# Kernel optimization log

Hardware: AMD Instinct MI355X
Metric: run time of the kernel (lower is better)

Reference implementation:

```python
import jax, jax.numpy as jnp
import numpy as np

W_BIT = 4
G_SIZE = 128
HID = 4096
INTER = 11008
TOKS = (2, 2048)


def _dequant(qw, qz, scales, g_size):
    """Unpack int4 nibbles from int32 and dequantize: (w - zero) * scale.
    qw: [K, N//8] int32, qz: [K//g, N//8] int32, scales: [K//g, N] float.
    Returns dense weight [K, N] in scales.dtype."""
    K = qw.shape[0]
    shifts = (jnp.arange(8, dtype=jnp.int32) * 4)  # 8 nibbles per int32
    w = ((qw[:, :, None] >> shifts) & 0xF).reshape(K, -1).astype(scales.dtype)   # [K, N]
    z = ((qz[:, :, None] >> shifts) & 0xF).reshape(qz.shape[0], -1).astype(scales.dtype)  # [K//g, N]
    zr = jnp.repeat(z, g_size, axis=0)       # broadcast zero-points over group rows
    sr = jnp.repeat(scales, g_size, axis=0)  # broadcast scales over group rows
    return (w - zr) * sr


def setup_inputs() -> dict:
    key = jax.random.key(0)
    ks = jax.random.split(key, 7)
    B, S = TOKS
    x = jax.random.normal(ks[0], (B, S, HID), dtype=jnp.float32)
    imax = 2147483647
    qweight_gu = jax.random.randint(ks[1], (HID, 2 * INTER // 8), 0, imax, dtype=jnp.int32)
    qzeros_gu = jax.random.randint(ks[2], (HID // G_SIZE, 2 * INTER // 8), 0, imax, dtype=jnp.int32)
    scales_gu = jax.random.uniform(ks[3], (HID // G_SIZE, 2 * INTER), dtype=jnp.float32) * 0.01 + 1e-3
    qweight_dn = jax.random.randint(ks[4], (INTER, HID // 8), 0, imax, dtype=jnp.int32)
    qzeros_dn = jax.random.randint(ks[5], (INTER // G_SIZE, HID // 8), 0, imax, dtype=jnp.int32)
    scales_dn = jax.random.uniform(ks[6], (INTER // G_SIZE, HID), dtype=jnp.float32) * 0.01 + 1e-3
    return {"x": x, "qweight_gu": qweight_gu, "qzeros_gu": qzeros_gu, "scales_gu": scales_gu,
            "qweight_dn": qweight_dn, "qzeros_dn": qzeros_dn, "scales_dn": scales_dn}


def reference(x, qweight_gu, qzeros_gu, scales_gu, qweight_dn, qzeros_dn, scales_dn):
    # gate_up projection: x [B,S,H] @ W_gu [H, 2*I]
    W_gu = _dequant(qweight_gu, qzeros_gu, scales_gu, G_SIZE)
    gate_up = jnp.einsum('bsh,hi->bsi', x, W_gu)
    d = gate_up.shape[-1] // 2
    # SiluAndMul: silu(gate) * up
    h = jax.nn.silu(gate_up[..., :d]) * gate_up[..., d:]
    # down projection: h [B,S,I] @ W_dn [I, H]
    W_dn = _dequant(qweight_dn, qzeros_dn, scales_dn, G_SIZE)
    return jnp.einsum('bsi,ih->bsh', h, W_dn)
```

## Files before the change

kernel.cpp:

```cpp
#include <hip/hip_runtime.h>
#include <hip/hip_bf16.h>
#include <hip/hip_fp16.h>
#include <cstdint>
#include <cstddef>

#define AS1 __attribute__((address_space(1)))
#define AS3 __attribute__((address_space(3)))

constexpr int HIDC   = 4096;
constexpr int INTERC = 11008;
constexpr int NTOKC  = 4096;
constexpr int NWGU   = 2 * INTERC;

using f32x4 = __attribute__((ext_vector_type(4))) float;
using f16x8 = __attribute__((ext_vector_type(8))) _Float16;


__global__ void cvt_x_kernel(const float4* __restrict__ x, ushort4* __restrict__ xh, int n4) {
  int stride = gridDim.x * blockDim.x;
  for (int i = blockIdx.x * blockDim.x + threadIdx.x; i < n4; i += stride) {
    float4 v = x[i];
    ushort4 o;
    o.x = __builtin_bit_cast(unsigned short, __float2half(v.x));
    o.y = __builtin_bit_cast(unsigned short, __float2half(v.y));
    o.z = __builtin_bit_cast(unsigned short, __float2half(v.z));
    o.w = __builtin_bit_cast(unsigned short, __float2half(v.w));
    xh[i] = o;
  }
}

__global__ void repack_kernel(const uint32_t* __restrict__ qw, uint32_t* __restrict__ qt,
                              int kints, int Wn) {
  long total  = (long)Wn * kints;
  long stride = (long)gridDim.x * blockDim.x;
  for (long idx = blockIdx.x * (long)blockDim.x + threadIdx.x; idx < total; idx += stride) {
    int col = (int)(idx / kints);
    int kk  = (int)(idx - (long)col * kints);
    uint32_t ow[8] = {0, 0, 0, 0, 0, 0, 0, 0};
#pragma unroll
    for (int j = 0; j < 8; ++j) {
      uint32_t v = qw[(size_t)(kk * 8 + j) * Wn + col];
      const int pos = (j & 1) ? (4 + (j >> 1)) : (j >> 1);
#pragma unroll
      for (int jn = 0; jn < 8; ++jn)
        ow[jn] |= ((v >> (4 * jn)) & 0xFu) << (4 * pos);
    }
#pragma unroll
    for (int jn = 0; jn < 8; ++jn)
      qt[(size_t)(col * 8 + jn) * kints + kk] = ow[jn];
  }
}

__global__ void mktab_kernel(const uint32_t* __restrict__ qz, const float* __restrict__ sc,
                             uint2* __restrict__ tab, int total, int Nw) {
  int stride = gridDim.x * blockDim.x;
  for (int idx = blockIdx.x * blockDim.x + threadIdx.x; idx < total; idx += stride) {
    int g = idx / Nw, n = idx - g * Nw;
    uint32_t z = (qz[(size_t)g * (Nw >> 3) + (n >> 3)] >> ((n & 7) * 4)) & 0xFu;
    float s = sc[idx];
    uint32_t us = (uint32_t)__builtin_bit_cast(unsigned short, __float2half(s));
    uint32_t uc = (uint32_t)__builtin_bit_cast(unsigned short, __float2half(-s * (float)z));
    tab[idx] = make_uint2(us | (us << 16), uc | (uc << 16));
  }
}

template <int DUAL, int NT, int KINTS, int NWTOT, int NXT, int K>
__global__ __launch_bounds__(512, 2) void qgemm_kernel(
    const __half* __restrict__ A, const uint32_t* __restrict__ QT,
    const uint2* __restrict__ TAB, __half* __restrict__ Hout,
    float* __restrict__ Fout) {
  __shared__ __align__(16) char lds[131072];

  const int tid  = threadIdx.x;
  const int lane = tid & 63;
  const int w    = tid >> 6;
  const int wr   = w >> 2, wc = w & 3;
  const int fr   = lane & 15;
  const int fq   = lane >> 4;

  const int nwg8 = (int)gridDim.x >> 3;
  const int g2   = (blockIdx.x & 7) * nwg8 + ((int)blockIdx.x >> 3);
  const int mt   = g2 / NXT;
  const int nt   = g2 - mt * NXT;
  const int row0 = mt * 256;

  int a_src[4];
#pragma unroll
  for (int i = 0; i < 4; ++i) {
    int o = i * 8192 + tid * 16;
    int r = o >> 7;
    int b = (o & 127) ^ ((r & 7) << 4);
    a_src[i] = (row0 + r) * K + (b >> 1);
  }

  const int tc = tid >> 1, kh = tid & 1;
  int wcol;
  if (DUAL) {
    const int p = tc >> 5, mat = (tc >> 4) & 1, c16 = tc & 15;
    wcol = nt * 128 + p * 16 + c16 + mat * INTERC;
  } else {
    wcol = nt * 256 + tc;
  }
  const uint32_t* qbase = QT + (size_t)wcol * KINTS + kh * 4;
  const int boff = 32768 + tc * 128;
  const int bswz = (tc & 7) << 4;

  f32x4 acc[8][4] = {};

  auto stageA = [&](int kt, int buf) {
#pragma unroll
    for (int i = 0; i < 4; ++i)
      __builtin_amdgcn_global_load_lds((const AS1 uint32_t*)(A + a_src[i] + kt * 64),
                                       (AS3 uint32_t*)(lds + buf * 65536 + i * 8192 + w * 1024),
                                       16, 0, 0);
  };

  auto dequantB = [&](uint4 q, uint2 tz, int buf) {
    const __half2 s2 = __builtin_bit_cast(__half2, tz.x);
    const __half2 c2 = __builtin_bit_cast(__half2, tz.y);
    const __half2 k1024 = __builtin_bit_cast(__half2, 0x64006400u);
    char* bd = lds + buf * 65536 + boff;
    uint32_t qq[4] = {q.x, q.y, q.z, q.w};
#pragma unroll
    for (int ii = 0; ii < 4; ++ii) {
      uint32_t r[4];
#pragma unroll
      for (int i = 0; i < 4; ++i) {
        uint32_t pr = ((qq[ii] >> (4 * i)) & 0x000F000Fu) | 0x64006400u;
        __half2 t  = __hsub2(__builtin_bit_cast(__half2, pr), k1024);
        __half2 wv = __hfma2(t, s2, c2);
        r[i] = __builtin_bit_cast(uint32_t, wv);
      }
      *(uint4*)(bd + ((kh * 64 + ii * 16) ^ bswz)) = make_uint4(r[0], r[1], r[2], r[3]);
    }
  };

  auto compute = [&](int buf) {
    const char* base = lds + buf * 65536;
#pragma unroll
    for (int kk = 0; kk < 2; ++kk) {
      const int bb = (((kk << 2) | fq) ^ (fr & 7)) << 4;
      f16x8 av[8], bv[4];
#pragma unroll
      for (int mi = 0; mi < 8; ++mi)
        av[mi] = *(const f16x8*)(base + (wr * 128 + mi * 16 + fr) * 128 + bb);
#pragma unroll
      for (int ni = 0; ni < 4; ++ni)
        bv[ni] = *(const f16x8*)(base + 32768 + (wc * 64 + ni * 16 + fr) * 128 + bb);
      __builtin_amdgcn_s_setprio(1);
#pragma unroll
      for (int mi = 0; mi < 8; ++mi)
#pragma unroll
        for (int ni = 0; ni < 4; ++ni)
          acc[mi][ni] = __builtin_amdgcn_mfma_f32_16x16x32_f16(av[mi], bv[ni], acc[mi][ni], 0, 0, 0);
      __builtin_amdgcn_s_setprio(0);
    }
  };

  uint4 q  = *(const uint4*)qbase;
  uint2 tz = TAB[(size_t)wcol];
  stageA(0, 0);
  dequantB(q, tz, 0);
  __syncthreads();
  q  = *(const uint4*)(qbase + 8);
  tz = TAB[(size_t)(1 >> 1) * NWTOT + wcol];

  int cur = 0;
#pragma unroll 1
  for (int kt = 0; kt < NT; ++kt) {
    if (kt + 1 < NT) {
      stageA(kt + 1, cur ^ 1);
      dequantB(q, tz, cur ^ 1);
    }
    if (kt + 2 < NT) {
      q  = *(const uint4*)(qbase + (kt + 2) * 8);
      tz = TAB[(size_t)((kt + 2) >> 1) * NWTOT + wcol];
    }
    compute(cur);
    __syncthreads();
    cur ^= 1;
  }

  if (DUAL) {
#pragma unroll
    for (int mi = 0; mi < 8; ++mi) {
      const int rr = row0 + wr * 128 + mi * 16 + fq * 4;
#pragma unroll
      for (int pp = 0; pp < 2; ++pp) {
        const int hcol = nt * 128 + (wc * 2 + pp) * 16 + fr;
#pragma unroll
        for (int r = 0; r < 4; ++r) {
          float gv = acc[mi][2 * pp][r];
          float uv = acc[mi][2 * pp + 1][r];
          float hv = gv / (1.0f + __expf(-gv)) * uv;
          Hout[(size_t)(rr + r) * INTERC + hcol] = __float2half(hv);
        }
      }
    }
  } else {
#pragma unroll
    for (int mi = 0; mi < 8; ++mi) {
      const int rr = row0 + wr * 128 + mi * 16 + fq * 4;
#pragma unroll
      for (int ni = 0; ni < 4; ++ni) {
        const int cc = nt * 256 + wc * 64 + ni * 16 + fr;
#pragma unroll
        for (int r = 0; r < 4; ++r)
          Fout[(size_t)(rr + r) * HIDC + cc] = acc[mi][ni][r];
      }
    }
  }
}

extern "C" void kernel_launch(void* const* d_in, const int* in_sizes, int n_in,
                              void* d_out, int out_size, void* d_ws, size_t ws_size,
                              hipStream_t stream) {
  const float*    x     = (const float*)d_in[0];
  const uint32_t* qw_gu = (const uint32_t*)d_in[1];
  const uint32_t* qz_gu = (const uint32_t*)d_in[2];
  const float*    sc_gu = (const float*)d_in[3];
  const uint32_t* qw_dn = (const uint32_t*)d_in[4];
  const uint32_t* qz_dn = (const uint32_t*)d_in[5];
  const float*    sc_dn = (const float*)d_in[6];
  float* out = (float*)d_out;

  char* ws = (char*)d_ws;
  __half*   xh   = (__half*)(ws + 0);
  uint32_t* qtgu = (uint32_t*)(ws + 33554432);
  uint32_t* qtdn = (uint32_t*)(ws + 78643200);
  uint2*    tgu  = (uint2*)(ws + 101187584);
  uint2*    tdn  = (uint2*)(ws + 106823680);
  __half*   hbuf = (__half*)(ws + 109641728);

  cvt_x_kernel<<<2048, 256, 0, stream>>>((const float4*)x, (ushort4*)xh, NTOKC * HIDC / 4);
  repack_kernel<<<2048, 256, 0, stream>>>(qw_gu, qtgu, HIDC / 8, NWGU / 8);
  repack_kernel<<<2048, 256, 0, stream>>>(qw_dn, qtdn, INTERC / 8, HIDC / 8);
  mktab_kernel<<<1024, 256, 0, stream>>>(qz_gu, sc_gu, tgu, (HIDC / 128) * NWGU, NWGU);
  mktab_kernel<<<1024, 256, 0, stream>>>(qz_dn, sc_dn, tdn, (INTERC / 128) * HIDC, HIDC);

  qgemm_kernel<1, 64, 512, NWGU, 86, HIDC>
      <<<1376, 512, 0, stream>>>(xh, qtgu, tgu, hbuf, nullptr);
  qgemm_kernel<0, 172, 1376, HIDC, 16, INTERC>
      <<<256, 512, 0, stream>>>(hbuf, qtdn, tdn, nullptr, out);
}
```

Baseline: 1.328 ms.

## Pre-dequantize weights to fp16 in chunks and run pipelined plain fp16 GEMM

Replaces the in-loop int4 dequantization with a separate deq kernel. It writes transposed fp16 weight tiles to workspace, splitting gate_up into three column chunks so they fit. The GEMM then streams both A and B into LDS with global_load_lds. It interleaves partial B/A loads with half-tile MFMA groups, using explicit vmcnt waits and barriers. This removes VALU dequant work and extra table loads from the MFMA main loop, at the cost of much more HBM traffic for the fp16 weights. Launch bounds also drop to one block per CU.

```diff
diff --git a/kernel.cpp b/kernel.cpp
--- a/kernel.cpp
+++ b/kernel.cpp
@@ -10,7 +10,6 @@
 constexpr int HIDC   = 4096;
 constexpr int INTERC = 11008;
 constexpr int NTOKC  = 4096;
-constexpr int NWGU   = 2 * INTERC;
 
 using f32x4 = __attribute__((ext_vector_type(4))) float;
 using f16x8 = __attribute__((ext_vector_type(8))) _Float16;
@@ -29,156 +28,134 @@
   }
 }
 
-__global__ void repack_kernel(const uint32_t* __restrict__ qw, uint32_t* __restrict__ qt,
-                              int kints, int Wn) {
-  long total  = (long)Wn * kints;
-  long stride = (long)gridDim.x * blockDim.x;
-  for (long idx = blockIdx.x * (long)blockDim.x + threadIdx.x; idx < total; idx += stride) {
-    int col = (int)(idx / kints);
-    int kk  = (int)(idx - (long)col * kints);
-    uint32_t ow[8] = {0, 0, 0, 0, 0, 0, 0, 0};
-#pragma unroll
-    for (int j = 0; j < 8; ++j) {
-      uint32_t v = qw[(size_t)(kk * 8 + j) * Wn + col];
-      const int pos = (j & 1) ? (4 + (j >> 1)) : (j >> 1);
-#pragma unroll
-      for (int jn = 0; jn < 8; ++jn)
-        ow[jn] |= ((v >> (4 * jn)) & 0xFu) << (4 * pos);
-    }
-#pragma unroll
-    for (int jn = 0; jn < 8; ++jn)
-      qt[(size_t)(col * 8 + jn) * kints + kk] = ow[jn];
-  }
-}
-
-__global__ void mktab_kernel(const uint32_t* __restrict__ qz, const float* __restrict__ sc,
-                             uint2* __restrict__ tab, int total, int Nw) {
-  int stride = gridDim.x * blockDim.x;
-  for (int idx = blockIdx.x * blockDim.x + threadIdx.x; idx < total; idx += stride) {
-    int g = idx / Nw, n = idx - g * Nw;
-    uint32_t z = (qz[(size_t)g * (Nw >> 3) + (n >> 3)] >> ((n & 7) * 4)) & 0xFu;
-    float s = sc[idx];
-    uint32_t us = (uint32_t)__builtin_bit_cast(unsigned short, __float2half(s));
-    uint32_t uc = (uint32_t)__builtin_bit_cast(unsigned short, __float2half(-s * (float)z));
-    tab[idx] = make_uint2(us | (us << 16), uc | (uc << 16));
-  }
-}
-
-template <int DUAL, int NT, int KINTS, int NWTOT, int NXT, int K>
-__global__ __launch_bounds__(512, 2) void qgemm_kernel(
-    const __half* __restrict__ A, const uint32_t* __restrict__ QT,
-    const uint2* __restrict__ TAB, __half* __restrict__ Hout,
-    float* __restrict__ Fout) {
+template <int GU>
+__global__ void deq_kernel(const uint32_t* __restrict__ qw, const uint32_t* __restrict__ qz,
+                           const float* __restrict__ sc, __half* __restrict__ WT,
+                           int cbase, int K, int Wn8, int Nsc) {
+  __shared__ __align__(16) __half tile[64][32];
+  const int tid = threadIdx.x;
+  const int bx = blockIdx.x;
+  const int k0 = blockIdx.y * 32;
+  const int k  = tid & 31, ws = tid >> 5;
+  const int g  = (k0 + k) >> 7;
+  int wordidx, nbase, nploc0;
+  if (GU) {
+    const int n0p = cbase + bx * 64;
+    const int h0  = n0p >> 1;
+    const int mat = ws >> 2, wsq = ws & 3;
+    wordidx = (mat * INTERC + h0) / 8 + wsq;
+    nbase   = mat * INTERC + h0 + wsq * 8;
+    nploc0  = ((wsq >> 1) << 5) + mat * 16 + ((wsq & 1) << 3);
+  } else {
+    const int n0 = cbase + bx * 64;
+    wordidx = n0 / 8 + ws;
+    nbase   = n0 + ws * 8;
+    nploc0  = ws * 8;
+  }
+  uint32_t q  = qw[(size_t)(k0 + k) * Wn8 + wordidx];
+  uint32_t zw = qz[(size_t)g * Wn8 + wordidx];
+#pragma unroll
+  for (int j = 0; j < 8; ++j) {
+    float v = (float)((q >> (4 * j)) & 0xFu);
+    float z = (float)((zw >> (4 * j)) & 0xFu);
+    float s = sc[(size_t)g * Nsc + nbase + j];
+    tile[nploc0 + j][k] = __float2half((v - z) * s);
+  }
+  __syncthreads();
+  const int nl = tid >> 2, kc = (tid & 3) * 8;
+  uint4 vv = *(const uint4*)&tile[nl][kc];
+  *(uint4*)&WT[(size_t)(bx * 64 + nl) * K + k0 + kc] = vv;
+}
+
+template <int DUAL, int NT, int K>
+__global__ __launch_bounds__(512, 1) void qgemm_kernel(
+    const __half* __restrict__ A, const __half* __restrict__ B,
+    __half* __restrict__ Hout, float* __restrict__ Fout) {
   __shared__ __align__(16) char lds[131072];
-
   const int tid  = threadIdx.x;
   const int lane = tid & 63;
   const int w    = tid >> 6;
   const int wr   = w >> 2, wc = w & 3;
-  const int fr   = lane & 15;
-  const int fq   = lane >> 4;
-
-  const int nwg8 = (int)gridDim.x >> 3;
-  const int g2   = (blockIdx.x & 7) * nwg8 + ((int)blockIdx.x >> 3);
-  const int mt   = g2 / NXT;
-  const int nt   = g2 - mt * NXT;
-  const int row0 = mt * 256;
-
-  int a_src[4];
+  const int fr   = lane & 15, fq = lane >> 4;
+  const int nt   = blockIdx.x, mt = blockIdx.y;
+  const int row0 = mt * 256, col0 = nt * 256;
+
+  int a_src[4], b_src[4];
 #pragma unroll
   for (int i = 0; i < 4; ++i) {
     int o = i * 8192 + tid * 16;
     int r = o >> 7;
     int b = (o & 127) ^ ((r & 7) << 4);
     a_src[i] = (row0 + r) * K + (b >> 1);
-  }
-
-  const int tc = tid >> 1, kh = tid & 1;
-  int wcol;
-  if (DUAL) {
-    const int p = tc >> 5, mat = (tc >> 4) & 1, c16 = tc & 15;
-    wcol = nt * 128 + p * 16 + c16 + mat * INTERC;
-  } else {
-    wcol = nt * 256 + tc;
-  }
-  const uint32_t* qbase = QT + (size_t)wcol * KINTS + kh * 4;
-  const int boff = 32768 + tc * 128;
-  const int bswz = (tc & 7) << 4;
+    b_src[i] = (col0 + r) * K + (b >> 1);
+  }
 
   f32x4 acc[8][4] = {};
-
-  auto stageA = [&](int kt, int buf) {
-#pragma unroll
-    for (int i = 0; i < 4; ++i)
-      __builtin_amdgcn_global_load_lds((const AS1 uint32_t*)(A + a_src[i] + kt * 64),
-                                       (AS3 uint32_t*)(lds + buf * 65536 + i * 8192 + w * 1024),
-                                       16, 0, 0);
-  };
-
-  auto dequantB = [&](uint4 q, uint2 tz, int buf) {
-    const __half2 s2 = __builtin_bit_cast(__half2, tz.x);
-    const __half2 c2 = __builtin_bit_cast(__half2, tz.y);
-    const __half2 k1024 = __builtin_bit_cast(__half2, 0x64006400u);
-    char* bd = lds + buf * 65536 + boff;
-    uint32_t qq[4] = {q.x, q.y, q.z, q.w};
-#pragma unroll
-    for (int ii = 0; ii < 4; ++ii) {
-      uint32_t r[4];
-#pragma unroll
-      for (int i = 0; i < 4; ++i) {
-        uint32_t pr = ((qq[ii] >> (4 * i)) & 0x000F000Fu) | 0x64006400u;
-        __half2 t  = __hsub2(__builtin_bit_cast(__half2, pr), k1024);
-        __half2 wv = __hfma2(t, s2, c2);
-        r[i] = __builtin_bit_cast(uint32_t, wv);
-      }
-      *(uint4*)(bd + ((kh * 64 + ii * 16) ^ bswz)) = make_uint4(r[0], r[1], r[2], r[3]);
-    }
-  };
-
-  auto compute = [&](int buf) {
+  f16x8 av[4], bv0[4], bv1[4];
+
+  auto glA = [&](int i, int kt, int buf) {
+    __builtin_amdgcn_global_load_lds(
+        (const AS1 uint32_t*)(A + (size_t)a_src[i] + (size_t)kt * 64),
+        (AS3 uint32_t*)(lds + buf * 65536 + i * 8192 + w * 1024), 16, 0, 0);
+  };
+  auto glB = [&](int i, int kt, int buf) {
+    __builtin_amdgcn_global_load_lds(
+        (const AS1 uint32_t*)(B + (size_t)b_src[i] + (size_t)kt * 64),
+        (AS3 uint32_t*)(lds + buf * 65536 + 32768 + i * 8192 + w * 1024), 16, 0, 0);
+  };
+  auto rdA = [&](int buf, int mh, int kk) {
+    const int bb = (((kk << 2) | fq) ^ (fr & 7)) << 4;
     const char* base = lds + buf * 65536;
 #pragma unroll
-    for (int kk = 0; kk < 2; ++kk) {
-      const int bb = (((kk << 2) | fq) ^ (fr & 7)) << 4;
-      f16x8 av[8], bv[4];
-#pragma unroll
-      for (int mi = 0; mi < 8; ++mi)
-        av[mi] = *(const f16x8*)(base + (wr * 128 + mi * 16 + fr) * 128 + bb);
-#pragma unroll
-      for (int ni = 0; ni < 4; ++ni)
-        bv[ni] = *(const f16x8*)(base + 32768 + (wc * 64 + ni * 16 + fr) * 128 + bb);
-      __builtin_amdgcn_s_setprio(1);
-#pragma unroll
-      for (int mi = 0; mi < 8; ++mi)
-#pragma unroll
-        for (int ni = 0; ni < 4; ++ni)
-          acc[mi][ni] = __builtin_amdgcn_mfma_f32_16x16x32_f16(av[mi], bv[ni], acc[mi][ni], 0, 0, 0);
-      __builtin_amdgcn_s_setprio(0);
-    }
-  };
-
-  uint4 q  = *(const uint4*)qbase;
-  uint2 tz = TAB[(size_t)wcol];
-  stageA(0, 0);
-  dequantB(q, tz, 0);
-  __syncthreads();
-  q  = *(const uint4*)(qbase + 8);
-  tz = TAB[(size_t)(1 >> 1) * NWTOT + wcol];
-
-  int cur = 0;
+    for (int j = 0; j < 4; ++j)
+      av[j] = *(const f16x8*)(base + (wr * 128 + mh * 64 + j * 16 + fr) * 128 + bb);
+  };
+  auto rdB = [&](int buf, int kk, f16x8* dst) {
+    const int bb = (((kk << 2) | fq) ^ (fr & 7)) << 4;
+    const char* base = lds + buf * 65536 + 32768;
+#pragma unroll
+    for (int n = 0; n < 4; ++n)
+      dst[n] = *(const f16x8*)(base + (wc * 64 + n * 16 + fr) * 128 + bb);
+  };
+  auto mfma16 = [&](f16x8* bvp, int mh) {
+    __builtin_amdgcn_s_setprio(1);
+#pragma unroll
+    for (int j = 0; j < 4; ++j)
+#pragma unroll
+      for (int n = 0; n < 4; ++n)
+        acc[mh * 4 + j][n] =
+            __builtin_amdgcn_mfma_f32_16x16x32_f16(av[j], bvp[n], acc[mh * 4 + j][n], 0, 0, 0);
+    __builtin_amdgcn_s_setprio(0);
+  };
+
+  glB(0, 0, 0); glB(1, 0, 0); glB(2, 0, 0); glB(3, 0, 0);
+  glA(0, 0, 0); glA(2, 0, 0); glA(1, 0, 0); glA(3, 0, 0);
+  asm volatile("s_waitcnt vmcnt(2)" ::: "memory");
+  asm volatile("s_barrier" ::: "memory");
+
 #pragma unroll 1
   for (int kt = 0; kt < NT; ++kt) {
-    if (kt + 1 < NT) {
-      stageA(kt + 1, cur ^ 1);
-      dequantB(q, tz, cur ^ 1);
-    }
-    if (kt + 2 < NT) {
-      q  = *(const uint4*)(qbase + (kt + 2) * 8);
-      tz = TAB[(size_t)((kt + 2) >> 1) * NWTOT + wcol];
-    }
-    compute(cur);
-    __syncthreads();
-    cur ^= 1;
+    const int cur = kt & 1, nxt = cur ^ 1;
+    const bool stg = (kt + 1 < NT);
+    if (stg) { glB(0, kt + 1, nxt); glB(1, kt + 1, nxt); }
+    rdB(cur, 0, bv0);
+    rdA(cur, 0, 0);
+    mfma16(bv0, 0);
+    if (stg) { glB(2, kt + 1, nxt); glB(3, kt + 1, nxt); }
+    rdB(cur, 1, bv1);
+    rdA(cur, 0, 1);
+    mfma16(bv1, 0);
+    if (stg) asm volatile("s_waitcnt vmcnt(4)" ::: "memory");
+    else     asm volatile("s_waitcnt vmcnt(0)" ::: "memory");
+    asm volatile("s_barrier" ::: "memory");
+    if (stg) { glA(0, kt + 1, nxt); glA(2, kt + 1, nxt); }
+    rdA(cur, 1, 0);
+    mfma16(bv0, 1);
+    if (stg) { glA(1, kt + 1, nxt); glA(3, kt + 1, nxt); }
+    rdA(cur, 1, 1);
+    mfma16(bv1, 1);
+    if (stg) asm volatile("s_waitcnt vmcnt(2)" ::: "memory");
+    asm volatile("s_barrier" ::: "memory");
   }
 
   if (DUAL) {
@@ -225,21 +202,24 @@
   float* out = (float*)d_out;
 
   char* ws = (char*)d_ws;
-  __half*   xh   = (__half*)(ws + 0);
-  uint32_t* qtgu = (uint32_t*)(ws + 33554432);
-  uint32_t* qtdn = (uint32_t*)(ws + 78643200);
-  uint2*    tgu  = (uint2*)(ws + 101187584);
-  uint2*    tdn  = (uint2*)(ws + 106823680);
-  __half*   hbuf = (__half*)(ws + 109641728);
+  __half* xh   = (__half*)(ws);
+  __half* WT   = (__half*)(ws + 33554432);
+  __half* hbuf = (__half*)(ws + 96468992);
+  __half* WTdn = (__half*)(ws);
 
   cvt_x_kernel<<<2048, 256, 0, stream>>>((const float4*)x, (ushort4*)xh, NTOKC * HIDC / 4);
-  repack_kernel<<<2048, 256, 0, stream>>>(qw_gu, qtgu, HIDC / 8, NWGU / 8);
-  repack_kernel<<<2048, 256, 0, stream>>>(qw_dn, qtdn, INTERC / 8, HIDC / 8);
-  mktab_kernel<<<1024, 256, 0, stream>>>(qz_gu, sc_gu, tgu, (HIDC / 128) * NWGU, NWGU);
-  mktab_kernel<<<1024, 256, 0, stream>>>(qz_dn, sc_dn, tdn, (INTERC / 128) * HIDC, HIDC);
-
-  qgemm_kernel<1, 64, 512, NWGU, 86, HIDC>
-      <<<1376, 512, 0, stream>>>(xh, qtgu, tgu, hbuf, nullptr);
-  qgemm_kernel<0, 172, 1376, HIDC, 16, INTERC>
-      <<<256, 512, 0, stream>>>(hbuf, qtdn, tdn, nullptr, out);
-}
+
+  const int cb[3] = {0, 7680, 15360};
+  const int nc[3] = {7680, 7680, 6656};
+  for (int c = 0; c < 3; ++c) {
+    deq_kernel<1><<<dim3(nc[c] / 64, HIDC / 32), 256, 0, stream>>>(
+        qw_gu, qz_gu, sc_gu, WT, cb[c], HIDC, 2752, 22016);
+    qgemm_kernel<1, 64, HIDC><<<dim3(nc[c] / 256, NTOKC / 256), 512, 0, stream>>>(
+        xh, WT, hbuf + cb[c] / 2, nullptr);
+  }
+
+  deq_kernel<0><<<dim3(HIDC / 64, INTERC / 32), 256, 0, stream>>>(
+      qw_dn, qz_dn, sc_dn, WTdn, 0, INTERC, 512, HIDC);
+  qgemm_kernel<0, 172, INTERC><<<dim3(HIDC / 256, NTOKC / 256), 512, 0, stream>>>(
+      hbuf, WTdn, nullptr, out);
+}
```

Measured after the change: 1.101 ms. -17.1%, faster.
